# Kernel tuning notes

Hardware: AMD Instinct MI355X
Metric: run time of the kernel (lower is better)

## Reference

```python
import jax, jax.numpy as jnp
import numpy as np

B, N, H = 16, 1024, 4
CH = (64, 128, 256, 512)
KV = 960
EPS = 1e-5  # InstanceNorm2d default eps


def setup_inputs() -> dict:
    key = jax.random.key(0)
    ks = jax.random.split(key, 16)
    s = 0.02
    inp = {
        "emb1": jax.random.normal(ks[0], (B, N, CH[0]), jnp.float32),
        "emb2": jax.random.normal(ks[1], (B, N, CH[1]), jnp.float32),
        "emb3": jax.random.normal(ks[2], (B, N, CH[2]), jnp.float32),
        "emb4": jax.random.normal(ks[3], (B, N, CH[3]), jnp.float32),
        "emb_all": jax.random.normal(ks[4], (B, N, KV), jnp.float32),
        # per-head query weights (torch Linear weight layout [out, in])
        "Wq1": jax.random.normal(ks[5], (H, CH[0] // 4, CH[0] // 4), jnp.float32) * s,
        "Wq2": jax.random.normal(ks[6], (H, CH[1] // 4, CH[1] // 4), jnp.float32) * s,
        "Wq3": jax.random.normal(ks[7], (H, CH[2] // 4, CH[2] // 4), jnp.float32) * s,
        "Wq4": jax.random.normal(ks[8], (H, CH[3] // 4, CH[3] // 4), jnp.float32) * s,
        # NOTE: original forward only ever uses self.key[0] / self.value[0]
        "Wk": jax.random.normal(ks[9], (KV // 4, KV // 4), jnp.float32) * s,
        "Wv": jax.random.normal(ks[10], (KV // 4, KV // 4), jnp.float32) * s,
        "Wo1": jax.random.normal(ks[11], (CH[0], CH[0]), jnp.float32) * s,
        "Wo2": jax.random.normal(ks[12], (CH[1], CH[1]), jnp.float32) * s,
        "Wo3": jax.random.normal(ks[13], (CH[2], CH[2]), jnp.float32) * s,
        "Wo4": jax.random.normal(ks[14], (CH[3], CH[3]), jnp.float32) * s,
    }
    return inp


def _heads_from_all(x):
    # Reproduce the per-head channel regrouping of emb_all:
    # head h takes [16h:16(h+1)] of scale1, [32h:...] of scale2, etc. -> [B,H,N,240]
    b, n, _ = x.shape
    parts = [
        x[:, :, 0:64].reshape(b, n, H, 16),
        x[:, :, 64:192].reshape(b, n, H, 32),
        x[:, :, 192:448].reshape(b, n, H, 64),
        x[:, :, 448:960].reshape(b, n, H, 128),
    ]
    return jnp.concatenate(parts, axis=-1).transpose(0, 2, 1, 3)


def _scale_attn(emb, Wq, Wo, Kh, Vh):
    b, n, c = emb.shape
    d = c // H
    q = emb.reshape(b, n, H, d)
    # per-head linear (torch: x @ W.T): [B,H,N,d]
    Qh = jnp.einsum('bnhd,hed->bhne', q, Wq)
    # channel attention: Q^T K -> [B,H,d,240]
    scores = jnp.einsum('bhnd,bhnk->bhdk', Qh, Kh) / np.float32(np.sqrt(KV))
    # InstanceNorm2d over heads (per (b,h), normalize over last two dims, biased var)
    m = scores.mean(axis=(2, 3), keepdims=True)
    v = scores.var(axis=(2, 3), keepdims=True)
    probs = jax.nn.softmax((scores - m) / jnp.sqrt(v + EPS), axis=-1)
    # probs @ V^T -> [B,H,d,N]
    ctx = jnp.einsum('bhdk,bhnk->bhdn', probs, Vh)
    # permute(0,3,2,1) -> [B,N,d,H], flatten -> [B,N,c]
    ctx = ctx.transpose(0, 3, 2, 1).reshape(b, n, c)
    return jnp.einsum('bnc,ec->bne', ctx, Wo)


def reference(emb1, emb2, emb3, emb4, emb_all,
              Wq1, Wq2, Wq3, Wq4, Wk, Wv, Wo1, Wo2, Wo3, Wo4):
    heads = _heads_from_all(emb_all)  # [B,H,N,240]
    Kh = jnp.einsum('bhnd,ed->bhne', heads, Wk)
    Vh = jnp.einsum('bhnd,ed->bhne', heads, Wv)
    O1 = _scale_attn(emb1, Wq1, Wo1, Kh, Vh)
    O2 = _scale_attn(emb2, Wq2, Wo2, Kh, Vh)
    O3 = _scale_attn(emb3, Wq3, Wo3, Kh, Vh)
    O4 = _scale_attn(emb4, Wq4, Wo4, Kh, Vh)
    return (O1, O2, O3, O4)
```

## Files before the change

### kernel.cpp

```cpp
#include <hip/hip_runtime.h>
#include <hip/hip_bf16.h>
#include <math.h>

#define B_   16
#define N_   1024
#define H_   4
#define D240 240
#define SC_  57600

typedef unsigned short ushort;
typedef __attribute__((ext_vector_type(8))) short bf16x8;
typedef __attribute__((ext_vector_type(8))) unsigned short u16x8;
typedef __attribute__((ext_vector_type(4))) float f32x4;

__device__ __forceinline__ ushort f2b(float v) {
  __hip_bfloat16 h = __float2bfloat16(v);
  return *reinterpret_cast<ushort*>(&h);
}

__device__ __forceinline__ void gload16(const void* g, void* s) {
  __builtin_amdgcn_global_load_lds((const __attribute__((address_space(1))) void*)g,
                                   (__attribute__((address_space(3))) void*)s, 16, 0, 0);
}

__global__ __launch_bounds__(256) void conv_inputs(const float* __restrict__ emb_all,
                                                   const float* __restrict__ e1,
                                                   const float* __restrict__ e2,
                                                   const float* __restrict__ e3,
                                                   const float* __restrict__ e4,
                                                   ushort* __restrict__ heads,
                                                   ushort* __restrict__ embh) {
  const int bn = blockIdx.x;
  const int b = bn >> 10, n = bn & 1023;
  const int t = threadIdx.x;
  const int which = t >> 7;
  const int gg = t & 127;
  const int h = gg >> 5;
  const int k0 = (gg & 31) * 8;

  ushort* dst = (which ? embh : heads) + (((long)b * H_ + h) * N_ + n) * 256 + k0;

  float4 p0 = {0.f, 0.f, 0.f, 0.f}, p1 = {0.f, 0.f, 0.f, 0.f};
  if (k0 < 240) {
    const float* src;
    if (which == 0) {
      const float* ha = emb_all + (long)bn * 960;
      if (k0 < 16)       src = ha + h * 16 + k0;
      else if (k0 < 48)  src = ha + 64  + h * 32  + (k0 - 16);
      else if (k0 < 112) src = ha + 192 + h * 64  + (k0 - 48);
      else               src = ha + 448 + h * 128 + (k0 - 112);
    } else {
      if (k0 < 16)       src = e1 + (long)bn * 64  + h * 16  + k0;
      else if (k0 < 48)  src = e2 + (long)bn * 128 + h * 32  + (k0 - 16);
      else if (k0 < 112) src = e3 + (long)bn * 256 + h * 64  + (k0 - 48);
      else               src = e4 + (long)bn * 512 + h * 128 + (k0 - 112);
    }
    p0 = *(const float4*)src;
    p1 = *(const float4*)(src + 4);
  }
  u16x8 w;
  w[0] = f2b(p0.x); w[1] = f2b(p0.y); w[2] = f2b(p0.z); w[3] = f2b(p0.w);
  w[4] = f2b(p1.x); w[5] = f2b(p1.y); w[6] = f2b(p1.z); w[7] = f2b(p1.w);
  *(u16x8*)dst = w;
}

__global__ __launch_bounds__(256) void conv_weights(
    const float* __restrict__ Wk, const float* __restrict__ Wv,
    const float* __restrict__ q1, const float* __restrict__ q2,
    const float* __restrict__ q3, const float* __restrict__ q4,
    const float* __restrict__ o1, const float* __restrict__ o2,
    const float* __restrict__ o3, const float* __restrict__ o4,
    ushort* __restrict__ wts) {
  long i = (long)blockIdx.x * 256 + threadIdx.x;
  if (i >= 716800) return;
  float v = 0.f;
  if (i < 122880) {
    const float* src = (i < 61440) ? Wk : Wv;
    long j = (i < 61440) ? i : i - 61440;
    int r = j / 256, k = j % 256;
    if (k < 240) v = src[(long)r * 240 + k];
  } else if (i < 368640) {
    long j = i - 122880;
    int h = j / 61440; int rem = j % 61440;
    int r = rem / 256, k = rem % 256;
    int s = r < 16 ? 0 : r < 48 ? 1 : r < 112 ? 2 : 3;
    const int dss[4] = {16, 32, 64, 128};
    const int qf[4]  = {0, 16, 48, 112};
    const float* qs[4] = {q1, q2, q3, q4};
    int d = dss[s], off = qf[s];
    if (k >= off && k < off + d)
      v = qs[s][((long)(h * d + (r - off))) * d + (k - off)];
  } else {
    long j = i - 368640;
    int s = j < 4096 ? 0 : j < 20480 ? 1 : j < 86016 ? 2 : 3;
    const long base[4] = {0, 4096, 20480, 86016};
    const int cs[4] = {64, 128, 256, 512};
    const float* os[4] = {o1, o2, o3, o4};
    long rem = j - base[s];
    int c = cs[s], d = c >> 2;
    int e = rem / c, kk = rem % c;
    v = os[s][(long)e * c + (kk % d) * 4 + kk / d];
  }
  wts[i] = f2b(v);
}

__global__ __launch_bounds__(256) void mfma_abT(
    const ushort* __restrict__ A, long lda, long AsY, long AsZ,
    const ushort* __restrict__ Bm, long ldb, long BsY, long BsZ,
    void* __restrict__ Cv, long ldc, long CsY, long CsZ,
    int M, int Nn, int Npad, int K, float alpha, int c_bf16, int tilesN)
{
  A  += blockIdx.y * AsY + blockIdx.z * AsZ;
  Bm += blockIdx.y * BsY + blockIdx.z * BsZ;

  const int m0 = (blockIdx.x / tilesN) * 128;
  const int n0 = (blockIdx.x % tilesN) * 128;
  const int tid = threadIdx.x;
  const int l = tid & 63, w = tid >> 6;
  const int wy = w >> 1, wx = w & 1;

  __shared__ __align__(16) ushort As[128 * 32];
  __shared__ __align__(16) ushort Bs[128 * 32];

  f32x4 acc[4][4];
  #pragma unroll
  for (int i = 0; i < 4; ++i)
    #pragma unroll
    for (int j = 0; j < 4; ++j) acc[i][j] = (f32x4)0.f;

  const int srow = tid >> 2;
  const int skc  = (tid & 3) * 8;
  int ra0 = m0 + srow;      ra0 = ra0 < M  ? ra0 : M - 1;
  int ra1 = m0 + srow + 64; ra1 = ra1 < M  ? ra1 : M - 1;
  int rb0 = n0 + srow;      rb0 = rb0 < Nn ? rb0 : Nn - 1;
  int rb1 = n0 + srow + 64; rb1 = rb1 < Nn ? rb1 : Nn - 1;
  const ushort* a0 = A  + (long)ra0 * lda + skc;
  const ushort* a1 = A  + (long)ra1 * lda + skc;
  const ushort* b0 = Bm + (long)rb0 * ldb + skc;
  const ushort* b1 = Bm + (long)rb1 * ldb + skc;
  ushort* lA0 = As + srow * 32 + skc;
  ushort* lA1 = As + (srow + 64) * 32 + skc;
  ushort* lB0 = Bs + srow * 32 + skc;
  ushort* lB1 = Bs + (srow + 64) * 32 + skc;

  const ushort* arp = As + (wy * 64 + (l & 15)) * 32 + (l >> 4) * 8;
  const ushort* brp = Bs + (wx * 64 + (l & 15)) * 32 + (l >> 4) * 8;

  for (int k0 = 0; k0 < K; k0 += 32) {
    __syncthreads();
    gload16(a0 + k0, lA0);
    gload16(a1 + k0, lA1);
    gload16(b0 + k0, lB0);
    gload16(b1 + k0, lB1);
    __syncthreads();
    bf16x8 af[4], bfr[4];
    #pragma unroll
    for (int i = 0; i < 4; ++i) af[i]  = *(const bf16x8*)(arp + i * 512);
    #pragma unroll
    for (int j = 0; j < 4; ++j) bfr[j] = *(const bf16x8*)(brp + j * 512);
    #pragma unroll
    for (int i = 0; i < 4; ++i)
      #pragma unroll
      for (int j = 0; j < 4; ++j)
        acc[i][j] = __builtin_amdgcn_mfma_f32_16x16x32_bf16(af[i], bfr[j], acc[i][j], 0, 0, 0);
  }

  const int quad = l >> 4, lc = l & 15;
  if (c_bf16) {
    ushort* C = (ushort*)Cv + blockIdx.y * CsY + blockIdx.z * CsZ;
    #pragma unroll
    for (int i = 0; i < 4; ++i) {
      #pragma unroll
      for (int r = 0; r < 4; ++r) {
        int row = m0 + wy * 64 + i * 16 + quad * 4 + r;
        if (row >= M) continue;
        ushort* Cr = C + (long)row * ldc;
        #pragma unroll
        for (int j = 0; j < 4; ++j) {
          int col = n0 + wx * 64 + j * 16 + lc;
          if (col < Nn) Cr[col] = f2b(acc[i][j][r] * alpha);
          else if (col < Npad) Cr[col] = 0;
        }
      }
    }
  } else {
    float* C = (float*)Cv + blockIdx.y * CsY + blockIdx.z * CsZ;
    #pragma unroll
    for (int i = 0; i < 4; ++i) {
      #pragma unroll
      for (int r = 0; r < 4; ++r) {
        int row = m0 + wy * 64 + i * 16 + quad * 4 + r;
        if (row >= M) continue;
        float* Cr = C + (long)row * ldc;
        #pragma unroll
        for (int j = 0; j < 4; ++j) {
          int col = n0 + wx * 64 + j * 16 + lc;
          if (col < Nn) Cr[col] = acc[i][j][r] * alpha;
        }
      }
    }
  }
}

__global__ __launch_bounds__(256) void mfma_ctx(const ushort* __restrict__ V,
                                                const ushort* __restrict__ P,
                                                ushort* __restrict__ ctx2) {
  const int h = blockIdx.y, b = blockIdx.z;
  const ushort* A  = V + (((long)b * H_ + h) * 1024) * 256;
  const ushort* Bm = P + (((long)b * H_ + h) * 240) * 256;

  const int m0 = (blockIdx.x >> 1) * 128;
  const int n0 = (blockIdx.x & 1) * 128;
  const int tid = threadIdx.x;
  const int l = tid & 63, w = tid >> 6;
  const int wy = w >> 1, wx = w & 1;

  __shared__ __align__(16) ushort As[128 * 32];
  __shared__ __align__(16) ushort Bs[128 * 32];

  f32x4 acc[4][4];
  #pragma unroll
  for (int i = 0; i < 4; ++i)
    #pragma unroll
    for (int j = 0; j < 4; ++j) acc[i][j] = (f32x4)0.f;

  const int srow = tid >> 2;
  const int skc  = (tid & 3) * 8;
  int rb0 = n0 + srow;      rb0 = rb0 < 240 ? rb0 : 239;
  int rb1 = n0 + srow + 64; rb1 = rb1 < 240 ? rb1 : 239;
  const ushort* a0 = A  + (long)(m0 + srow) * 256 + skc;
  const ushort* a1 = A  + (long)(m0 + srow + 64) * 256 + skc;
  const ushort* b0 = Bm + (long)rb0 * 256 + skc;
  const ushort* b1 = Bm + (long)rb1 * 256 + skc;
  ushort* lA0 = As + srow * 32 + skc;
  ushort* lA1 = As + (srow + 64) * 32 + skc;
  ushort* lB0 = Bs + srow * 32 + skc;
  ushort* lB1 = Bs + (srow + 64) * 32 + skc;

  const ushort* arp = As + (wy * 64 + (l & 15)) * 32 + (l >> 4) * 8;
  const ushort* brp = Bs + (wx * 64 + (l & 15)) * 32 + (l >> 4) * 8;

  for (int k0 = 0; k0 < 256; k0 += 32) {
    __syncthreads();
    gload16(a0 + k0, lA0);
    gload16(a1 + k0, lA1);
    gload16(b0 + k0, lB0);
    gload16(b1 + k0, lB1);
    __syncthreads();
    bf16x8 af[4], bfr[4];
    #pragma unroll
    for (int i = 0; i < 4; ++i) af[i]  = *(const bf16x8*)(arp + i * 512);
    #pragma unroll
    for (int j = 0; j < 4; ++j) bfr[j] = *(const bf16x8*)(brp + j * 512);
    #pragma unroll
    for (int i = 0; i < 4; ++i)
      #pragma unroll
      for (int j = 0; j < 4; ++j)
        acc[i][j] = __builtin_amdgcn_mfma_f32_16x16x32_bf16(af[i], bfr[j], acc[i][j], 0, 0, 0);
  }

  const int quad = l >> 4, lc = l & 15;
  const int dss[4] = {16, 32, 64, 128};
  const int qf[4]  = {0, 16, 48, 112};
  const int cf[4]  = {0, 64, 192, 448};
  #pragma unroll
  for (int i = 0; i < 4; ++i) {
    #pragma unroll
    for (int r = 0; r < 4; ++r) {
      int row = m0 + wy * 64 + i * 16 + quad * 4 + r;
      ushort* Cr = ctx2 + ((long)b * N_ + row) * 960;
      #pragma unroll
      for (int j = 0; j < 4; ++j) {
        int col = n0 + wx * 64 + j * 16 + lc;
        if (col < 240) {
          int s = col < 16 ? 0 : col < 48 ? 1 : col < 112 ? 2 : 3;
          int chan = cf[s] + h * dss[s] + (col - qf[s]);
          Cr[chan] = f2b(acc[i][j][r]);
        }
      }
    }
  }
}

__global__ __launch_bounds__(256) void mfma_oproj(const ushort* __restrict__ ctx2,
                                                  const ushort* __restrict__ Wo_b,
                                                  float* __restrict__ out) {
  const int bx = blockIdx.x;
  int s = bx < 128 ? 0 : bx < 256 ? 1 : bx < 512 ? 2 : 3;
  const int sbase[4] = {0, 128, 256, 512};
  const int cs_[4]   = {64, 128, 256, 512};
  const int coff_[4] = {0, 64, 192, 448};
  const int wo_[4]   = {0, 4096, 20480, 86016};
  const long oo_[4]  = {0, 1048576, 3145728, 7340032};
  const int c = cs_[s];
  const int nt = (c + 127) >> 7;
  const int local = bx - sbase[s];
  const int m0 = (local / nt) * 128;
  const int n0 = (local % nt) * 128;

  const ushort* A  = ctx2 + coff_[s];
  const ushort* Bm = Wo_b + wo_[s];
  float* C = out + oo_[s];
  const int K = c, Nn = c;

  const int tid = threadIdx.x;
  const int l = tid & 63, w = tid >> 6;
  const int wy = w >> 1, wx = w & 1;

  __shared__ __align__(16) ushort As[128 * 32];
  __shared__ __align__(16) ushort Bs[128 * 32];

  f32x4 acc[4][4];
  #pragma unroll
  for (int i = 0; i < 4; ++i)
    #pragma unroll
    for (int j = 0; j < 4; ++j) acc[i][j] = (f32x4)0.f;

  const int srow = tid >> 2;
  const int skc  = (tid & 3) * 8;
  int rb0 = n0 + srow;      rb0 = rb0 < Nn ? rb0 : Nn - 1;
  int rb1 = n0 + srow + 64; rb1 = rb1 < Nn ? rb1 : Nn - 1;
  const ushort* a0 = A  + (long)(m0 + srow) * 960 + skc;
  const ushort* a1 = A  + (long)(m0 + srow + 64) * 960 + skc;
  const ushort* b0 = Bm + (long)rb0 * c + skc;
  const ushort* b1 = Bm + (long)rb1 * c + skc;
  ushort* lA0 = As + srow * 32 + skc;
  ushort* lA1 = As + (srow + 64) * 32 + skc;
  ushort* lB0 = Bs + srow * 32 + skc;
  ushort* lB1 = Bs + (srow + 64) * 32 + skc;

  const ushort* arp = As + (wy * 64 + (l & 15)) * 32 + (l >> 4) * 8;
  const ushort* brp = Bs + (wx * 64 + (l & 15)) * 32 + (l >> 4) * 8;

  for (int k0 = 0; k0 < K; k0 += 32) {
    __syncthreads();
    gload16(a0 + k0, lA0);
    gload16(a1 + k0, lA1);
    gload16(b0 + k0, lB0);
    gload16(b1 + k0, lB1);
    __syncthreads();
    bf16x8 af[4], bfr[4];
    #pragma unroll
    for (int i = 0; i < 4; ++i) af[i]  = *(const bf16x8*)(arp + i * 512);
    #pragma unroll
    for (int j = 0; j < 4; ++j) bfr[j] = *(const bf16x8*)(brp + j * 512);
    #pragma unroll
    for (int i = 0; i < 4; ++i)
      #pragma unroll
      for (int j = 0; j < 4; ++j)
        acc[i][j] = __builtin_amdgcn_mfma_f32_16x16x32_bf16(af[i], bfr[j], acc[i][j], 0, 0, 0);
  }

  const int quad = l >> 4, lc = l & 15;
  #pragma unroll
  for (int i = 0; i < 4; ++i) {
    #pragma unroll
    for (int r = 0; r < 4; ++r) {
      int row = m0 + wy * 64 + i * 16 + quad * 4 + r;
      float* Cr = C + (long)row * c;
      #pragma unroll
      for (int j = 0; j < 4; ++j) {
        int col = n0 + wx * 64 + j * 16 + lc;
        if (col < Nn) Cr[col] = acc[i][j][r];
      }
    }
  }
}

__global__ __launch_bounds__(256) void in_stats(const float* __restrict__ sc,
                                                float* __restrict__ stats) {
  const int doffs[4] = {0, 16, 48, 112};
  const int dss[4]   = {16, 32, 64, 128};
  const int bh = blockIdx.x, sidx = blockIdx.y;
  const float4* S4 = (const float4*)(sc + (long)bh * SC_ + doffs[sidx] * D240);
  const int n4 = dss[sidx] * 60;

  float s = 0.f, s2 = 0.f;
  for (int i = threadIdx.x; i < n4; i += 256) {
    float4 v = S4[i];
    s  += v.x + v.y + v.z + v.w;
    s2 += v.x * v.x + v.y * v.y + v.z * v.z + v.w * v.w;
  }
  #pragma unroll
  for (int o = 32; o > 0; o >>= 1) { s += __shfl_down(s, o); s2 += __shfl_down(s2, o); }

  __shared__ float wsum[4], wsum2[4];
  const int wave = threadIdx.x >> 6, lane = threadIdx.x & 63;
  if (lane == 0) { wsum[wave] = s; wsum2[wave] = s2; }
  __syncthreads();
  if (threadIdx.x == 0) {
    float n = (float)(n4 * 4);
    float ts = wsum[0] + wsum[1] + wsum[2] + wsum[3];
    float ts2 = wsum2[0] + wsum2[1] + wsum2[2] + wsum2[3];
    float mean = ts / n;
    float var = ts2 / n - mean * mean;
    stats[(bh * 4 + sidx) * 2]     = mean;
    stats[(bh * 4 + sidx) * 2 + 1] = rsqrtf(var + 1e-5f);
  }
}

__global__ __launch_bounds__(256) void sm_apply(const float* __restrict__ sc,
                                                const float* __restrict__ stats,
                                                ushort* __restrict__ P) {
  const int bh = blockIdx.y;
  const int row = blockIdx.x * 4 + (threadIdx.x >> 6);
  const int lane = threadIdx.x & 63;
  const int s = row < 16 ? 0 : row < 48 ? 1 : row < 112 ? 2 : 3;
  const float mean = stats[(bh * 4 + s) * 2];
  const float rstd = stats[(bh * 4 + s) * 2 + 1];
  const float* r = sc + (long)bh * SC_ + (long)row * D240;
  ushort* p = P + ((long)bh * D240 + row) * 256;

  float v[4];
  float mx = -1e30f;
  #pragma unroll
  for (int j = 0; j < 4; ++j) {
    int c = lane + j * 64;
    v[j] = (c < D240) ? (r[c] - mean) * rstd : -1e30f;
    mx = fmaxf(mx, v[j]);
  }
  #pragma unroll
  for (int o = 32; o > 0; o >>= 1) mx = fmaxf(mx, __shfl_xor(mx, o));
  float sum = 0.f;
  #pragma unroll
  for (int j = 0; j < 4; ++j) {
    int c = lane + j * 64;
    v[j] = (c < D240) ? __expf(v[j] - mx) : 0.f;
    sum += v[j];
  }
  #pragma unroll
  for (int o = 32; o > 0; o >>= 1) sum += __shfl_xor(sum, o);
  float inv = 1.f / sum;
  #pragma unroll
  for (int j = 0; j < 4; ++j) {
    int c = lane + j * 64;
    p[c] = (c < D240) ? f2b(v[j] * inv) : (ushort)0;
  }
}

extern "C" void kernel_launch(void* const* d_in, const int* in_sizes, int n_in,
                              void* d_out, int out_size, void* d_ws, size_t ws_size,
                              hipStream_t stream) {
  const float* emb[4] = {(const float*)d_in[0], (const float*)d_in[1],
                         (const float*)d_in[2], (const float*)d_in[3]};
  const float* emb_all = (const float*)d_in[4];
  const float* Wq[4] = {(const float*)d_in[5], (const float*)d_in[6],
                        (const float*)d_in[7], (const float*)d_in[8]};
  const float* Wk = (const float*)d_in[9];
  const float* Wv = (const float*)d_in[10];
  const float* Wo[4] = {(const float*)d_in[11], (const float*)d_in[12],
                        (const float*)d_in[13], (const float*)d_in[14]};
  float* out = (float*)d_out;
  float* sc  = (float*)d_out;

  ushort* wsb     = (ushort*)d_ws;
  ushort* heads_b = wsb;
  ushort* ctx2    = wsb;
  ushort* emb_h   = wsb + 16777216;
  ushort* P_b     = wsb + 16777216;
  ushort* Q_T     = wsb + 33554432;
  ushort* Kh_T    = wsb + 49283072;
  ushort* Vh      = wsb + 65011712;
  ushort* wts     = wsb + 81788928;
  ushort* Wk_b  = wts;
  ushort* Wv_b  = wts + 61440;
  ushort* Wq_bd = wts + 122880;
  ushort* Wo_b  = wts + 368640;
  float*  stats = (float*)(wsb + 82505728);

  const long sbh256 = 1024L * 256;
  const float alpha_s = 1.0f / sqrtf(960.0f);

  conv_inputs<<<dim3(B_ * N_), 256, 0, stream>>>(emb_all, emb[0], emb[1], emb[2], emb[3],
                                                 heads_b, emb_h);
  conv_weights<<<dim3(2800), 256, 0, stream>>>(Wk, Wv, Wq[0], Wq[1], Wq[2], Wq[3],
                                               Wo[0], Wo[1], Wo[2], Wo[3], wts);

  mfma_abT<<<dim3(16, 64, 1), 256, 0, stream>>>(
      Wk_b, 256, 0, 0,
      heads_b, 256, sbh256, 0,
      Kh_T, 1024, 240L * 1024, 0,
      240, 1024, 1024, 256, 1.f, 1, 8);

  mfma_abT<<<dim3(16, 64, 1), 256, 0, stream>>>(
      heads_b, 256, sbh256, 0,
      Wv_b, 256, 0, 0,
      Vh, 256, sbh256, 0,
      1024, 240, 256, 256, 1.f, 1, 2);

  mfma_abT<<<dim3(16, H_, B_), 256, 0, stream>>>(
      Wq_bd, 256, 240L * 256, 0,
      emb_h, 256, sbh256, (long)H_ * sbh256,
      Q_T, 1024, 240L * 1024, 4L * 240 * 1024,
      240, 1024, 1024, 256, 1.f, 1, 8);

  mfma_abT<<<dim3(4, 64, 1), 256, 0, stream>>>(
      Q_T, 1024, 240L * 1024, 0,
      Kh_T, 1024, 240L * 1024, 0,
      sc, 240, (long)SC_, 0,
      240, 240, 240, 1024, alpha_s, 0, 2);

  in_stats<<<dim3(64, 4), 256, 0, stream>>>(sc, stats);
  sm_apply<<<dim3(60, 64), 256, 0, stream>>>(sc, stats, P_b);

  mfma_ctx<<<dim3(16, H_, B_), 256, 0, stream>>>(Vh, P_b, ctx2);

  mfma_oproj<<<dim3(1024), 256, 0, stream>>>(ctx2, Wo_b, out);
}
```

Baseline: 367.1 us.

## Merge projection GEMMs into one launch and split-K the score GEMM

The three separate K, V and Q projection GEMM launches become a single mfma_proj kernel that dispatches by block index, removing launch gaps and tail underutilisation. The score GEMM (K=1024, only 256 blocks) is split into two K-halves written to two partial buffers, doubling parallelism. The stats and softmax kernels sum the two partials on load. conv_inputs now handles 8 rows per block, using fewer blocks. The split-K adds extra fp32 partial traffic and reuses output memory as scratch.

Result: faster. 349.7 us (-4.7%).

```diff
diff --git a/kernel.cpp b/kernel.cpp
--- a/kernel.cpp
+++ b/kernel.cpp
@@ -30,38 +30,45 @@
                                                    const float* __restrict__ e4,
                                                    ushort* __restrict__ heads,
                                                    ushort* __restrict__ embh) {
-  const int bn = blockIdx.x;
-  const int b = bn >> 10, n = bn & 1023;
   const int t = threadIdx.x;
   const int which = t >> 7;
   const int gg = t & 127;
   const int h = gg >> 5;
   const int k0 = (gg & 31) * 8;
-
-  ushort* dst = (which ? embh : heads) + (((long)b * H_ + h) * N_ + n) * 256 + k0;
-
-  float4 p0 = {0.f, 0.f, 0.f, 0.f}, p1 = {0.f, 0.f, 0.f, 0.f};
-  if (k0 < 240) {
-    const float* src;
-    if (which == 0) {
-      const float* ha = emb_all + (long)bn * 960;
-      if (k0 < 16)       src = ha + h * 16 + k0;
-      else if (k0 < 48)  src = ha + 64  + h * 32  + (k0 - 16);
-      else if (k0 < 112) src = ha + 192 + h * 64  + (k0 - 48);
-      else               src = ha + 448 + h * 128 + (k0 - 112);
-    } else {
-      if (k0 < 16)       src = e1 + (long)bn * 64  + h * 16  + k0;
-      else if (k0 < 48)  src = e2 + (long)bn * 128 + h * 32  + (k0 - 16);
-      else if (k0 < 112) src = e3 + (long)bn * 256 + h * 64  + (k0 - 48);
-      else               src = e4 + (long)bn * 512 + h * 128 + (k0 - 112);
+  const bool active = (k0 < 240);
+
+  const float* base;
+  int stride;
+  long soff;
+  if (which == 0) {
+    base = emb_all; stride = 960;
+    if (k0 < 16)       soff = h * 16 + k0;
+    else if (k0 < 48)  soff = 64  + h * 32  + (k0 - 16);
+    else if (k0 < 112) soff = 192 + h * 64  + (k0 - 48);
+    else               soff = 448 + h * 128 + (k0 - 112);
+  } else {
+    if (k0 < 16)       { base = e1; stride = 64;  soff = h * 16  + k0; }
+    else if (k0 < 48)  { base = e2; stride = 128; soff = h * 32  + (k0 - 16); }
+    else if (k0 < 112) { base = e3; stride = 256; soff = h * 64  + (k0 - 48); }
+    else               { base = e4; stride = 512; soff = h * 128 + (k0 - 112); }
+  }
+  ushort* dbase = which ? embh : heads;
+
+  #pragma unroll
+  for (int i = 0; i < 8; ++i) {
+    const int bn = blockIdx.x * 8 + i;
+    const int b = bn >> 10, n = bn & 1023;
+    float4 p0 = {0.f, 0.f, 0.f, 0.f}, p1 = {0.f, 0.f, 0.f, 0.f};
+    if (active) {
+      const float* s = base + (long)bn * stride + soff;
+      p0 = *(const float4*)s;
+      p1 = *(const float4*)(s + 4);
     }
-    p0 = *(const float4*)src;
-    p1 = *(const float4*)(src + 4);
-  }
-  u16x8 w;
-  w[0] = f2b(p0.x); w[1] = f2b(p0.y); w[2] = f2b(p0.z); w[3] = f2b(p0.w);
-  w[4] = f2b(p1.x); w[5] = f2b(p1.y); w[6] = f2b(p1.z); w[7] = f2b(p1.w);
-  *(u16x8*)dst = w;
+    u16x8 w;
+    w[0] = f2b(p0.x); w[1] = f2b(p0.y); w[2] = f2b(p0.z); w[3] = f2b(p0.w);
+    w[4] = f2b(p1.x); w[5] = f2b(p1.y); w[6] = f2b(p1.z); w[7] = f2b(p1.w);
+    *(u16x8*)(dbase + (((long)b * H_ + h) * N_ + n) * 256 + k0) = w;
+  }
 }
 
 __global__ __launch_bounds__(256) void conv_weights(
@@ -104,6 +111,116 @@
   wts[i] = f2b(v);
 }
 
+__device__ __forceinline__ void gemm_core_b16(
+    ushort* As, ushort* Bs,
+    const ushort* __restrict__ A, long lda,
+    const ushort* __restrict__ Bm, long ldb,
+    ushort* __restrict__ C, long ldc,
+    int M, int Nn, int Npad, int K, int m0, int n0)
+{
+  const int tid = threadIdx.x;
+  const int l = tid & 63, w = tid >> 6;
+  const int wy = w >> 1, wx = w & 1;
+
+  f32x4 acc[4][4];
+  #pragma unroll
+  for (int i = 0; i < 4; ++i)
+    #pragma unroll
+    for (int j = 0; j < 4; ++j) acc[i][j] = (f32x4)0.f;
+
+  const int srow = tid >> 2;
+  const int skc  = (tid & 3) * 8;
+  int ra0 = m0 + srow;      ra0 = ra0 < M  ? ra0 : M - 1;
+  int ra1 = m0 + srow + 64; ra1 = ra1 < M  ? ra1 : M - 1;
+  int rb0 = n0 + srow;      rb0 = rb0 < Nn ? rb0 : Nn - 1;
+  int rb1 = n0 + srow + 64; rb1 = rb1 < Nn ? rb1 : Nn - 1;
+  const ushort* a0 = A  + (long)ra0 * lda + skc;
+  const ushort* a1 = A  + (long)ra1 * lda + skc;
+  const ushort* b0 = Bm + (long)rb0 * ldb + skc;
+  const ushort* b1 = Bm + (long)rb1 * ldb + skc;
+  ushort* lA0 = As + srow * 32 + skc;
+  ushort* lA1 = As + (srow + 64) * 32 + skc;
+  ushort* lB0 = Bs + srow * 32 + skc;
+  ushort* lB1 = Bs + (srow + 64) * 32 + skc;
+
+  const ushort* arp = As + (wy * 64 + (l & 15)) * 32 + (l >> 4) * 8;
+  const ushort* brp = Bs + (wx * 64 + (l & 15)) * 32 + (l >> 4) * 8;
+
+  for (int k0 = 0; k0 < K; k0 += 32) {
+    __syncthreads();
+    gload16(a0 + k0, lA0);
+    gload16(a1 + k0, lA1);
+    gload16(b0 + k0, lB0);
+    gload16(b1 + k0, lB1);
+    __syncthreads();
+    bf16x8 af[4], bfr[4];
+    #pragma unroll
+    for (int i = 0; i < 4; ++i) af[i]  = *(const bf16x8*)(arp + i * 512);
+    #pragma unroll
+    for (int j = 0; j < 4; ++j) bfr[j] = *(const bf16x8*)(brp + j * 512);
+    #pragma unroll
+    for (int i = 0; i < 4; ++i)
+      #pragma unroll
+      for (int j = 0; j < 4; ++j)
+        acc[i][j] = __builtin_amdgcn_mfma_f32_16x16x32_bf16(af[i], bfr[j], acc[i][j], 0, 0, 0);
+  }
+
+  const int quad = l >> 4, lc = l & 15;
+  #pragma unroll
+  for (int i = 0; i < 4; ++i) {
+    #pragma unroll
+    for (int r = 0; r < 4; ++r) {
+      int row = m0 + wy * 64 + i * 16 + quad * 4 + r;
+      if (row >= M) continue;
+      ushort* Cr = C + (long)row * ldc;
+      #pragma unroll
+      for (int j = 0; j < 4; ++j) {
+        int col = n0 + wx * 64 + j * 16 + lc;
+        if (col < Nn) Cr[col] = f2b(acc[i][j][r]);
+        else if (col < Npad) Cr[col] = 0;
+      }
+    }
+  }
+}
+
+__global__ __launch_bounds__(256) void mfma_proj(
+    const ushort* __restrict__ heads_b, const ushort* __restrict__ emb_h,
+    const ushort* __restrict__ Wk_b, const ushort* __restrict__ Wv_b,
+    const ushort* __restrict__ Wq_bd,
+    ushort* __restrict__ Kh_T, ushort* __restrict__ Vh, ushort* __restrict__ Q_T)
+{
+  __shared__ __align__(16) ushort As[128 * 32];
+  __shared__ __align__(16) ushort Bs[128 * 32];
+  const int bx = blockIdx.x;
+  const long sbh = 1024L * 256;
+
+  if (bx < 1024) {
+    const int bh = bx >> 4, t = bx & 15;
+    gemm_core_b16(As, Bs,
+                  Wk_b, 256,
+                  heads_b + (long)bh * sbh, 256,
+                  Kh_T + (long)bh * 240 * 1024, 1024,
+                  240, 1024, 1024, 256, (t >> 3) * 128, (t & 7) * 128);
+  } else if (bx < 2048) {
+    const int local = bx - 1024;
+    const int bh = local >> 4, t = local & 15;
+    gemm_core_b16(As, Bs,
+                  heads_b + (long)bh * sbh, 256,
+                  Wv_b, 256,
+                  Vh + (long)bh * sbh, 256,
+                  1024, 240, 256, 256, (t >> 1) * 128, (t & 1) * 128);
+  } else {
+    const int local = bx - 2048;
+    const int bh = local >> 4, t = local & 15;
+    const int h = bh & 3;
+    gemm_core_b16(As, Bs,
+                  Wq_bd + h * 61440, 256,
+                  emb_h + (long)bh * sbh, 256,
+                  Q_T + (long)bh * 240 * 1024, 1024,
+                  240, 1024, 1024, 256, (t >> 3) * 128, (t & 7) * 128);
+  }
+}
+
 __global__ __launch_bounds__(256) void mfma_abT(
     const ushort* __restrict__ A, long lda, long AsY, long AsZ,
     const ushort* __restrict__ Bm, long ldb, long BsY, long BsZ,
@@ -367,19 +484,23 @@
   }
 }
 
-__global__ __launch_bounds__(256) void in_stats(const float* __restrict__ sc,
+__global__ __launch_bounds__(256) void in_stats(const float* __restrict__ sc0,
+                                                const float* __restrict__ sc1,
                                                 float* __restrict__ stats) {
   const int doffs[4] = {0, 16, 48, 112};
   const int dss[4]   = {16, 32, 64, 128};
   const int bh = blockIdx.x, sidx = blockIdx.y;
-  const float4* S4 = (const float4*)(sc + (long)bh * SC_ + doffs[sidx] * D240);
+  const long base = (long)bh * SC_ + doffs[sidx] * D240;
+  const float4* A4 = (const float4*)(sc0 + base);
+  const float4* B4 = (const float4*)(sc1 + base);
   const int n4 = dss[sidx] * 60;
 
   float s = 0.f, s2 = 0.f;
   for (int i = threadIdx.x; i < n4; i += 256) {
-    float4 v = S4[i];
-    s  += v.x + v.y + v.z + v.w;
-    s2 += v.x * v.x + v.y * v.y + v.z * v.z + v.w * v.w;
+    float4 a = A4[i], b = B4[i];
+    float x0 = a.x + b.x, x1 = a.y + b.y, x2 = a.z + b.z, x3 = a.w + b.w;
+    s  += x0 + x1 + x2 + x3;
+    s2 += x0 * x0 + x1 * x1 + x2 * x2 + x3 * x3;
   }
   #pragma unroll
   for (int o = 32; o > 0; o >>= 1) { s += __shfl_down(s, o); s2 += __shfl_down(s2, o); }
@@ -399,7 +520,8 @@
   }
 }
 
-__global__ __launch_bounds__(256) void sm_apply(const float* __restrict__ sc,
+__global__ __launch_bounds__(256) void sm_apply(const float* __restrict__ sc0,
+                                                const float* __restrict__ sc1,
                                                 const float* __restrict__ stats,
                                                 ushort* __restrict__ P) {
   const int bh = blockIdx.y;
@@ -408,7 +530,9 @@
   const int s = row < 16 ? 0 : row < 48 ? 1 : row < 112 ? 2 : 3;
   const float mean = stats[(bh * 4 + s) * 2];
   const float rstd = stats[(bh * 4 + s) * 2 + 1];
-  const float* r = sc + (long)bh * SC_ + (long)row * D240;
+  const long base = (long)bh * SC_ + (long)row * D240;
+  const float* r0 = sc0 + base;
+  const float* r1 = sc1 + base;
   ushort* p = P + ((long)bh * D240 + row) * 256;
 
   float v[4];
@@ -416,7 +540,7 @@
   #pragma unroll
   for (int j = 0; j < 4; ++j) {
     int c = lane + j * 64;
-    v[j] = (c < D240) ? (r[c] - mean) * rstd : -1e30f;
+    v[j] = (c < D240) ? (r0[c] + r1[c] - mean) * rstd : -1e30f;
     mx = fmaxf(mx, v[j]);
   }
   #pragma unroll
@@ -451,7 +575,8 @@
   const float* Wo[4] = {(const float*)d_in[11], (const float*)d_in[12],
                         (const float*)d_in[13], (const float*)d_in[14]};
   float* out = (float*)d_out;
-  float* sc  = (float*)d_out;
+  float* sc0 = (float*)d_out;
+  float* sc1 = (float*)d_out + 64L * SC_;
 
   ushort* wsb     = (ushort*)d_ws;
   ushort* heads_b = wsb;
@@ -468,40 +593,24 @@
   ushort* Wo_b  = wts + 368640;
   float*  stats = (float*)(wsb + 82505728);
 
-  const long sbh256 = 1024L * 256;
   const float alpha_s = 1.0f / sqrtf(960.0f);
 
-  conv_inputs<<<dim3(B_ * N_), 256, 0, stream>>>(emb_all, emb[0], emb[1], emb[2], emb[3],
-                                                 heads_b, emb_h);
   conv_weights<<<dim3(2800), 256, 0, stream>>>(Wk, Wv, Wq[0], Wq[1], Wq[2], Wq[3],
                                                Wo[0], Wo[1], Wo[2], Wo[3], wts);
-
-  mfma_abT<<<dim3(16, 64, 1), 256, 0, stream>>>(
-      Wk_b, 256, 0, 0,
-      heads_b, 256, sbh256, 0,
-      Kh_T, 1024, 240L * 1024, 0,
-      240, 1024, 1024, 256, 1.f, 1, 8);
-
-  mfma_abT<<<dim3(16, 64, 1), 256, 0, stream>>>(
-      heads_b, 256, sbh256, 0,
-      Wv_b, 256, 0, 0,
-      Vh, 256, sbh256, 0,
-      1024, 240, 256, 256, 1.f, 1, 2);
-
-  mfma_abT<<<dim3(16, H_, B_), 256, 0, stream>>>(
-      Wq_bd, 256, 240L * 256, 0,
-      emb_h, 256, sbh256, (long)H_ * sbh256,
-      Q_T, 1024, 240L * 1024, 4L * 240 * 1024,
-      240, 1024, 1024, 256, 1.f, 1, 8);
-
-  mfma_abT<<<dim3(4, 64, 1), 256, 0, stream>>>(
-      Q_T, 1024, 240L * 1024, 0,
-      Kh_T, 1024, 240L * 1024, 0,
-      sc, 240, (long)SC_, 0,
-      240, 240, 240, 1024, alpha_s, 0, 2);
-
-  in_stats<<<dim3(64, 4), 256, 0, stream>>>(sc, stats);
-  sm_apply<<<dim3(60, 64), 256, 0, stream>>>(sc, stats, P_b);
+  conv_inputs<<<dim3(2048), 256, 0, stream>>>(emb_all, emb[0], emb[1], emb[2], emb[3],
+                                              heads_b, emb_h);
+
+  mfma_proj<<<dim3(3072), 256, 0, stream>>>(heads_b, emb_h, Wk_b, Wv_b, Wq_bd,
+                                            Kh_T, Vh, Q_T);
+
+  mfma_abT<<<dim3(4, 64, 2), 256, 0, stream>>>(
+      Q_T, 1024, 240L * 1024, 512,
+      Kh_T, 1024, 240L * 1024, 512,
+      sc0, 240, (long)SC_, 64L * SC_,
+      240, 240, 240, 512, alpha_s, 0, 2);
+
+  in_stats<<<dim3(64, 4), 256, 0, stream>>>(sc0, sc1, stats);
+  sm_apply<<<dim3(60, 64), 256, 0, stream>>>(sc0, sc1, stats, P_b);
 
   mfma_ctx<<<dim3(16, H_, B_), 256, 0, stream>>>(Vh, P_b, ctx2);
 
```
